# Kernel tuning notes

Hardware: AMD Instinct MI355X
Metric: run time of the kernel (lower is better)

Reference implementation:

```python
import jax, jax.numpy as jnp
import numpy as np

GRID_ROWS, GRID_COLS = 7, 10
GRID_SIZE = GRID_ROWS * GRID_COLS  # 70
CONTEXT_SIZE = 24
STATE_SIZE = GRID_SIZE + CONTEXT_SIZE  # 94
H = 128  # LSTM_HIDDEN


def setup_inputs() -> dict:
    key = jax.random.key(0)
    ks = jax.random.split(key, 16)
    B, T = 1024, 128
    inp = {
        'states_seq': jax.random.normal(ks[0], (B, T, STATE_SIZE), jnp.float32),
        'actions_seq': jax.random.randint(ks[1], (B, T), 0, 4).astype(jnp.int32),
        # conv params (OIHW)
        'conv1_w': jax.random.normal(ks[2], (16, 1, 3, 3), jnp.float32) * 0.3,
        'conv1_b': jnp.zeros((16,), jnp.float32),
        'conv2_w': jax.random.normal(ks[3], (32, 16, 3, 3), jnp.float32) * 0.08,
        'conv2_b': jnp.zeros((32,), jnp.float32),
        # dense params (out, in) like torch Linear
        'grid_fc_w': jax.random.normal(ks[4], (128, 32 * GRID_SIZE), jnp.float32) * 0.02,
        'grid_fc_b': jnp.zeros((128,), jnp.float32),
        'ctx_fc_w': jax.random.normal(ks[5], (64, CONTEXT_SIZE), jnp.float32) * 0.2,
        'ctx_fc_b': jnp.zeros((64,), jnp.float32),
        'trunk_w': jax.random.normal(ks[6], (128, 192), jnp.float32) * 0.07,
        'trunk_b': jnp.zeros((128,), jnp.float32),
        # LSTM params
        'W_ih': jax.random.normal(ks[7], (4 * H, 128), jnp.float32) * 0.09,
        'b_ih': jnp.zeros((4 * H,), jnp.float32),
        'W_hh': jax.random.normal(ks[8], (4 * H, H), jnp.float32) * 0.09,
        # heads
        'actor_w': jax.random.uniform(ks[9], (4, H), jnp.float32, -0.01, 0.01),
        'actor_b': jnp.zeros((4,), jnp.float32),
        'critic_w': jax.random.uniform(ks[10], (1, H), jnp.float32, -0.01, 0.01),
        'critic_b': jnp.zeros((1,), jnp.float32),
    }
    return inp


def _forward(states_seq, actions_seq, conv1_w, conv1_b, conv2_w, conv2_b,
             grid_fc_w, grid_fc_b, ctx_fc_w, ctx_fc_b, trunk_w, trunk_b,
             W_ih, b_ih, W_hh, actor_w, actor_b, critic_w, critic_b):
    B, T, _ = states_seq.shape
    x = states_seq.reshape(-1, STATE_SIZE)                  # (N, 94)
    grid = x[:, :GRID_SIZE].reshape(-1, 1, GRID_ROWS, GRID_COLS)
    ctx = x[:, GRID_SIZE:]
    g = jax.lax.conv_general_dilated(grid, conv1_w, (1, 1), 'SAME',
                                     dimension_numbers=('NCHW', 'OIHW', 'NCHW'))
    g = jax.nn.relu(g + conv1_b[None, :, None, None])
    g = jax.lax.conv_general_dilated(g, conv2_w, (1, 1), 'SAME',
                                     dimension_numbers=('NCHW', 'OIHW', 'NCHW'))
    g = jax.nn.relu(g + conv2_b[None, :, None, None])
    g = g.reshape(g.shape[0], -1)                           # (N, 2240)
    g = jax.nn.relu(g @ grid_fc_w.T + grid_fc_b)            # (N, 128)
    c = jax.nn.relu(ctx @ ctx_fc_w.T + ctx_fc_b)            # (N, 64)
    trunk = jax.nn.relu(jnp.concatenate([g, c], -1) @ trunk_w.T + trunk_b)
    trunk = trunk.reshape(B, T, 128)

    # LSTM: precompute input-to-gate GEMM for all timesteps, scan over time
    gates_x = jnp.einsum('btd,gd->tbg', trunk, W_ih) + b_ih  # (T, B, 4H)

    def step(carry, gx):
        h, cst = carry
        gates = gx + h @ W_hh.T
        i, f, gg, o = jnp.split(gates, 4, axis=-1)
        i, f, o = jax.nn.sigmoid(i), jax.nn.sigmoid(f), jax.nn.sigmoid(o)
        gg = jnp.tanh(gg)
        cst = f * cst + i * gg
        h = o * jnp.tanh(cst)
        return (h, cst), h

    h0 = jnp.zeros((B, H), trunk.dtype)
    _, hs = jax.lax.scan(step, (h0, h0), gates_x)            # hs: (T, B, H)
    h_flat = jnp.transpose(hs, (1, 0, 2)).reshape(B * T, H)

    logits = h_flat @ actor_w.T + actor_b                    # (N, 4)
    values = (h_flat @ critic_w.T + critic_b)[:, 0]          # (N,)
    logp = jax.nn.log_softmax(logits, axis=-1)
    a = actions_seq.reshape(-1)
    log_probs = jnp.take_along_axis(logp, a[:, None].astype(jnp.int32), axis=-1)[:, 0]
    entropy = -jnp.sum(jnp.exp(logp) * logp, axis=-1)
    return log_probs, values, entropy


def reference(states_seq, actions_seq, conv1_w, conv1_b, conv2_w, conv2_b,
              grid_fc_w, grid_fc_b, ctx_fc_w, ctx_fc_b, trunk_w, trunk_b,
              W_ih, b_ih, W_hh, actor_w, actor_b, critic_w, critic_b):
    return _forward(states_seq, actions_seq, conv1_w, conv1_b, conv2_w, conv2_b,
                    grid_fc_w, grid_fc_b, ctx_fc_w, ctx_fc_b, trunk_w, trunk_b,
                    W_ih, b_ih, W_hh, actor_w, actor_b, critic_w, critic_b)
```

## Files before the change

### kernel.cpp

```cpp
#include <hip/hip_runtime.h>
#include <hip/hip_bf16.h>

typedef unsigned int  u32;
typedef unsigned short u16;
typedef unsigned long long u64;
typedef __attribute__((ext_vector_type(8))) short bf16x8;
typedef __attribute__((ext_vector_type(4))) float f32x4;

#define B_   1024
#define T_   128
#define NBT  (B_*T_)
#define CHUNK 32768
#define NCHUNK 4

#define WG_OFF   0
#define WT_OFF   286720
#define WIH_OFF  311296
#define W2_OFF   376832
#define W1C_OFF  381952
#define CVT_TOTAL 382464

#define TRUNK_OFF (1ull<<20)
#define H_OFF     (36ull<<20)
#define CTX_OFF   (72ull<<20)
#define C2_OFF    (92ull<<20)
#define GX_OFF    C2_OFF

__device__ __forceinline__ u16 f2bf(float f){
  __hip_bfloat16 h = __float2bfloat16(f);
  return *reinterpret_cast<u16*>(&h);
}
__device__ __forceinline__ float bf2f(u16 u){ return __uint_as_float((u32)u << 16); }
__device__ __forceinline__ float sigm(float x){ return 1.f / (1.f + __expf(-x)); }
__device__ __forceinline__ float tanh_f(float x){ return 2.f / (1.f + __expf(-2.f*x)) - 1.f; }

__device__ __forceinline__ void bar_lds() {
  __builtin_amdgcn_sched_barrier(0);
  asm volatile("s_waitcnt lgkmcnt(0)" ::: "memory");
  __builtin_amdgcn_s_barrier();
  __builtin_amdgcn_sched_barrier(0);
}

__global__ void k_cvt(const float* __restrict__ gfw, const float* __restrict__ tw,
                      const float* __restrict__ wih, const float* __restrict__ c2w,
                      const float* __restrict__ c1w, u16* __restrict__ wsb) {
  int i = blockIdx.x * 256 + threadIdx.x;
  if (i >= CVT_TOTAL) return;
  float v;
  if (i < WT_OFF) {
    int o = i / 2240; int k = i - o*2240;
    int pos = k >> 5, ch = k & 31;
    v = gfw[o*2240 + ch*70 + pos];
  }
  else if (i < WIH_OFF)  v = tw[i - WT_OFF];
  else if (i < W2_OFF)   v = wih[i - WIH_OFF];
  else if (i < W1C_OFF) {
    int j = i - W2_OFF; int co = j / 160; int k = j - co*160;
    int tap = k >> 4; int ci = k & 15;
    v = (tap < 9) ? c2w[co*144 + ci*9 + tap] : 0.f;
  } else {
    int j = i - W1C_OFF; int ch = j >> 5; int k = j & 31;
    v = (k < 9) ? c1w[ch*9 + k] : 0.f;
  }
  wsb[i] = f2bf(v);
}

__global__ __launch_bounds__(512, 4) void k_conv(
    const float* __restrict__ states,
    const float* __restrict__ c1b, const float* __restrict__ c2b,
    const float* __restrict__ cfw, const float* __restrict__ cfb,
    const u16* __restrict__ wsb,
    u16* __restrict__ c2g,
    u16* __restrict__ ctxg)
{
  __shared__ float s_st[8][96];
  __shared__ __align__(16) u16 act1[8*108*16];

  const int tid  = threadIdx.x;
  const int lane = tid & 63;
  const int w    = tid >> 6;
  const int arow = lane & 15;
  const int grp  = lane >> 4;
  const int g0   = blockIdx.x * 64;

  bf16x8 Bc1 = *(const bf16x8*)(wsb + W1C_OFF + arow*32 + grp*8);
  bf16x8 b2f[5][2];
  #pragma unroll
  for (int p = 0; p < 5; p++)
    #pragma unroll
    for (int nt = 0; nt < 2; nt++)
      b2f[p][nt] = *(const bf16x8*)(wsb + W2_OFF + (nt*16 + arow)*160 + p*32 + grp*8);
  float c1bv[4], c2bv0[4], c2bv1[4];
  #pragma unroll
  for (int r = 0; r < 4; r++) {
    c1bv[r]  = c1b[grp*4 + r];
    c2bv0[r] = c2b[grp*4 + r];
    c2bv1[r] = c2b[16 + grp*4 + r];
  }
  const float cfbr = cfb[lane];
  float cfwr[24];
  #pragma unroll
  for (int k = 0; k < 24; k++) cfwr[k] = cfw[lane*24 + k];

  const int sst_s = (tid*2)/94, sst_c = (tid*2)%94;

  if (tid < 376) {
    float2 v = *(const float2*)(states + (size_t)g0*94 + tid*2);
    *(float2*)&s_st[sst_s][sst_c] = v;
  }
  for (int i = tid; i < 608; i += 512) {
    int s = i / 76; int r = i - s*76; int hi2 = r >> 1; int h = r & 1;
    int hp;
    if (hi2 < 12)      hp = hi2;
    else if (hi2 < 24) hp = 96 + (hi2 - 12);
    else if (hi2 < 31) hp = (hi2 - 23) * 12;
    else               hp = (hi2 - 30) * 12 + 11;
    u32 a = (u32)((s*108 + hp)*32 + h*16) ^ (u32)((hp & 7) << 4);
    *(uint4*)((char*)act1 + a) = (uint4){0,0,0,0};
  }
  bar_lds();

  const bf16x8 zv = {0,0,0,0,0,0,0,0};

  for (int g = 0; g < 8; g++) {
    const int m0 = g0 + g*8;
    float2 npre;
    const bool haspre = (g < 7) && (tid < 376);
    if (haspre)
      npre = *(const float2*)(states + (size_t)(m0 + 8)*94 + tid*2);

    for (int mt = w; mt < 35; mt += 8) {
      int row = mt*16 + arow;
      int s = (int)(((u32)row * 59919u) >> 22); int pos = row - s*70;
      int y = (int)(((u32)pos * 6554u) >> 16);  int x = pos - y*10;
      bf16x8 pf = zv;
      if (grp == 0) {
        const float* gs = &s_st[s][0];
        #pragma unroll
        for (int t = 0; t < 8; t++) {
          int dy = t/3, dx = t - (t/3)*3;
          int yy = y + dy - 1, xx = x + dx - 1;
          bool ok = (yy >= 0) & (yy < 7) & (xx >= 0) & (xx < 10);
          float v = gs[ok ? yy*10 + xx : 0];
          pf[t] = (short)f2bf(ok ? v : 0.f);
        }
      } else if (grp == 1) {
        int yy = y + 1, xx = x + 1;
        bool ok = (yy < 7) & (xx < 10);
        float v = s_st[s][ok ? yy*10 + xx : 0];
        pf[0] = (short)f2bf(ok ? v : 0.f);
      }
      f32x4 acc = __builtin_amdgcn_mfma_f32_16x16x32_bf16(Bc1, pf, (f32x4){0.f,0.f,0.f,0.f}, 0, 0, 0);
      int hp = (y+1)*12 + (x+1);
      u16 q0 = f2bf(fmaxf(acc[0] + c1bv[0], 0.f));
      u16 q1 = f2bf(fmaxf(acc[1] + c1bv[1], 0.f));
      u16 q2 = f2bf(fmaxf(acc[2] + c1bv[2], 0.f));
      u16 q3 = f2bf(fmaxf(acc[3] + c1bv[3], 0.f));
      u64 pk = (u64)q0 | ((u64)q1 << 16) | ((u64)q2 << 32) | ((u64)q3 << 48);
      u32 wa = (u32)(((s*108 + hp)*16 + grp*4)*2) ^ (u32)((hp & 7) << 4);
      *(u64*)((char*)act1 + wa) = pk;
    }
    bar_lds();

    for (int mt = w; mt < 35; mt += 8) {
      int row = mt*16 + arow;
      int s = (int)(((u32)row * 59919u) >> 22); int pos = row - s*70;
      int y = (int)(((u32)pos * 6554u) >> 16);  int x = pos - y*10;
      f32x4 acc0 = {0.f,0.f,0.f,0.f}, acc1 = {0.f,0.f,0.f,0.f};
      #pragma unroll
      for (int p = 0; p < 5; p++) {
        int tap = p*2 + (grp >> 1); if (tap > 8) tap = 8;
        int dy = (tap * 11) >> 5; int dx = tap - dy*3;
        int hp = (y + dy)*12 + (x + dx);
        u32 ra = (u32)(((s*108 + hp)*16 + (grp & 1)*8)*2) ^ (u32)((hp & 7) << 4);
        bf16x8 bv = *(const bf16x8*)((const char*)act1 + ra);
        acc0 = __builtin_amdgcn_mfma_f32_16x16x32_bf16(b2f[p][0], bv, acc0, 0, 0, 0);
        acc1 = __builtin_amdgcn_mfma_f32_16x16x32_bf16(b2f[p][1], bv, acc1, 0, 0, 0);
      }
      {
        u16 q0 = f2bf(fmaxf(acc0[0] + c2bv0[0], 0.f));
        u16 q1 = f2bf(fmaxf(acc0[1] + c2bv0[1], 0.f));
        u16 q2 = f2bf(fmaxf(acc0[2] + c2bv0[2], 0.f));
        u16 q3 = f2bf(fmaxf(acc0[3] + c2bv0[3], 0.f));
        u64 pk = (u64)q0 | ((u64)q1 << 16) | ((u64)q2 << 32) | ((u64)q3 << 48);
        *(u64*)(c2g + (size_t)(m0 + s)*2240 + pos*32 + grp*4) = pk;
      }
      {
        u16 q0 = f2bf(fmaxf(acc1[0] + c2bv1[0], 0.f));
        u16 q1 = f2bf(fmaxf(acc1[1] + c2bv1[1], 0.f));
        u16 q2 = f2bf(fmaxf(acc1[2] + c2bv1[2], 0.f));
        u16 q3 = f2bf(fmaxf(acc1[3] + c2bv1[3], 0.f));
        u64 pk = (u64)q0 | ((u64)q1 << 16) | ((u64)q2 << 32) | ((u64)q3 << 48);
        *(u64*)(c2g + (size_t)(m0 + s)*2240 + pos*32 + 16 + grp*4) = pk;
      }
    }
    {
      float a = cfbr;
      #pragma unroll
      for (int k = 0; k < 24; k++) a = fmaf(cfwr[k], s_st[w][70 + k], a);
      ctxg[(size_t)(m0 + w)*64 + lane] = f2bf(fmaxf(a, 0.f));
    }

    if (g < 7) {
      bar_lds();
      if (haspre) *(float2*)&s_st[sst_s][sst_c] = npre;
      bar_lds();
    }
  }
}

__global__ __launch_bounds__(512, 2) void k_gemm(
    const u16* __restrict__ c2g, const u16* __restrict__ ctxg,
    const float* __restrict__ gfb, const float* __restrict__ tbv,
    const u16* __restrict__ wsb, u16* __restrict__ trunk_ws, int nbase)
{
  __shared__ __align__(16) u16 s_b[2][128*72];
  __shared__ __align__(16) u16 s_g[64*204];

  const int tid  = threadIdx.x;
  const int lane = tid & 63;
  const int w    = tid >> 6;
  const int arow = lane & 15;
  const int grp  = lane >> 4;
  const int wm   = w & 3;
  const int wn   = w >> 2;
  const int m0   = blockIdx.x * 64;

  float gfbv[4], tbvv[4];
  #pragma unroll
  for (int q = 0; q < 4; q++) {
    gfbv[q] = gfb[(wn*4 + q)*16 + arow];
    tbvv[q] = tbv[(wn*4 + q)*16 + arow];
  }

  const int srow = tid >> 2, sseg = (tid & 3) * 16;
  const u16* wg = wsb + WG_OFF;
  const u16* ap = c2g + (size_t)(m0 + wm*16 + arow) * 2240 + grp*8;

  {
    const u16* src = wg + (size_t)srow*2240 + sseg;
    *(uint4*)&s_b[0][srow*72 + sseg]     = *(const uint4*)src;
    *(uint4*)&s_b[0][srow*72 + sseg + 8] = *(const uint4*)(src + 8);
  }
  bf16x8 aC0 = *(const bf16x8*)(ap);
  bf16x8 aC1 = *(const bf16x8*)(ap + 32);
  bf16x8 aN0 = *(const bf16x8*)(ap + 64);
  bf16x8 aN1 = *(const bf16x8*)(ap + 96);
  f32x4 acc[4];
  #pragma unroll
  for (int q = 0; q < 4; q++) acc[q] = (f32x4){0.f,0.f,0.f,0.f};
  __syncthreads();

  for (int kp = 0; kp < 35; kp++) {
    uint4 b0v, b1v;
    if (kp < 34) {
      const u16* src = wg + (size_t)srow*2240 + (kp+1)*64 + sseg;
      b0v = *(const uint4*)src;
      b1v = *(const uint4*)(src + 8);
    }
    bf16x8 aF0 = aN0, aF1 = aN1;
    if (kp < 33) {
      aF0 = *(const bf16x8*)(ap + (size_t)(kp+2)*64);
      aF1 = *(const bf16x8*)(ap + (size_t)(kp+2)*64 + 32);
    }
    const u16* sb = &s_b[kp & 1][0];
    #pragma unroll
    for (int q = 0; q < 4; q++) {
      bf16x8 bv0 = *(const bf16x8*)&sb[((wn*4 + q)*16 + arow)*72 + grp*8];
      acc[q] = __builtin_amdgcn_mfma_f32_16x16x32_bf16(aC0, bv0, acc[q], 0, 0, 0);
    }
    #pragma unroll
    for (int q = 0; q < 4; q++) {
      bf16x8 bv1 = *(const bf16x8*)&sb[((wn*4 + q)*16 + arow)*72 + 32 + grp*8];
      acc[q] = __builtin_amdgcn_mfma_f32_16x16x32_bf16(aC1, bv1, acc[q], 0, 0, 0);
    }
    if (kp < 34) {
      *(uint4*)&s_b[(kp+1) & 1][srow*72 + sseg]     = b0v;
      *(uint4*)&s_b[(kp+1) & 1][srow*72 + sseg + 8] = b1v;
    }
    aC0 = aN0; aC1 = aN1; aN0 = aF0; aN1 = aF1;
    bar_lds();
  }

  #pragma unroll
  for (int q = 0; q < 4; q++)
    #pragma unroll
    for (int r = 0; r < 4; r++)
      s_g[(wm*16 + grp*4 + r)*204 + (wn*4 + q)*16 + arow] = f2bf(fmaxf(acc[q][r] + gfbv[q], 0.f));
  {
    int row = tid >> 3, seg = (tid & 7) * 8;
    uint4 c0 = *(const uint4*)(ctxg + (size_t)(m0 + row)*64 + seg);
    *(uint4*)&s_g[row*204 + 128 + seg] = c0;
  }
  bar_lds();

  f32x4 tacc[4];
  #pragma unroll
  for (int q = 0; q < 4; q++) tacc[q] = (f32x4){0.f,0.f,0.f,0.f};
  #pragma unroll
  for (int ks = 0; ks < 6; ks++) {
    bf16x8 av = *(const bf16x8*)&s_g[(wm*16 + arow)*204 + ks*32 + grp*8];
    #pragma unroll
    for (int q = 0; q < 4; q++) {
      bf16x8 bv = *(const bf16x8*)(wsb + WT_OFF + (size_t)((wn*4 + q)*16 + arow)*192 + ks*32 + grp*8);
      tacc[q] = __builtin_amdgcn_mfma_f32_16x16x32_bf16(av, bv, tacc[q], 0, 0, 0);
    }
  }
  bar_lds();
  #pragma unroll
  for (int q = 0; q < 4; q++)
    #pragma unroll
    for (int r = 0; r < 4; r++)
      s_g[(wm*16 + grp*4 + r)*204 + (wn*4 + q)*16 + arow] = f2bf(fmaxf(tacc[q][r] + tbvv[q], 0.f));
  bar_lds();

  {
    const int t0 = (nbase + m0) & 127;
    const int bb = (nbase + m0) >> 7;
    int row = tid >> 3, seg = (tid & 7) * 16;
    #pragma unroll
    for (int j = 0; j < 2; j++) {
      uint4 v = *(const uint4*)&s_g[row*204 + seg + j*8];
      *(uint4*)(trunk_ws + ((size_t)(t0 + row)*B_ + bb)*128 + seg + j*8) = v;
    }
  }
}

__global__ __launch_bounds__(512, 2) void k_xg(
    const u16* __restrict__ trunk_ws, const u16* __restrict__ wsb,
    u16* __restrict__ gxg)
{
  const int tid  = threadIdx.x;
  const int lane = tid & 63;
  const int w    = tid >> 6;
  const int arow = lane & 15;
  const int grp  = lane >> 4;
  const int t    = blockIdx.x >> 3;
  const int bch  = (blockIdx.x & 7) * 128;
  const int samp = bch + w*16 + arow;

  bf16x8 bv[4];
  #pragma unroll
  for (int ks = 0; ks < 4; ks++)
    bv[ks] = *(const bf16x8*)(trunk_ws + ((size_t)t*B_ + samp)*128 + ks*32 + grp*8);

  const u16* wip = wsb + WIH_OFF;
  u16* gout = gxg + ((size_t)t*B_ + samp)*512;

  #pragma unroll 1
  for (int ntb = 0; ntb < 32; ntb += 4) {
    f32x4 acc[4];
    #pragma unroll
    for (int q = 0; q < 4; q++) acc[q] = (f32x4){0.f,0.f,0.f,0.f};
    #pragma unroll
    for (int ks = 0; ks < 4; ks++) {
      #pragma unroll
      for (int q = 0; q < 4; q++) {
        bf16x8 aw = *(const bf16x8*)(wip + (size_t)((ntb+q)*16 + arow)*128 + ks*32 + grp*8);
        acc[q] = __builtin_amdgcn_mfma_f32_16x16x32_bf16(aw, bv[ks], acc[q], 0, 0, 0);
      }
    }
    #pragma unroll
    for (int q = 0; q < 4; q++) {
      u16 q0 = f2bf(acc[q][0]);
      u16 q1 = f2bf(acc[q][1]);
      u16 q2 = f2bf(acc[q][2]);
      u16 q3 = f2bf(acc[q][3]);
      u64 pk = (u64)q0 | ((u64)q1 << 16) | ((u64)q2 << 32) | ((u64)q3 << 48);
      *(u64*)(gout + (ntb+q)*16 + grp*4) = pk;
    }
  }
}

__global__ __launch_bounds__(512, 1) void k_lstm(
    const u16* __restrict__ gxg, const float* __restrict__ whh,
    const float* __restrict__ bih, u16* __restrict__ h_ws)
{
  __shared__ __align__(16) u16 s_h[2][16*136];

  const int tid  = threadIdx.x;
  const int lane = tid & 63;
  const int w    = tid >> 6;
  const int arow = lane & 15;
  const int grp  = lane >> 4;
  const int b0   = blockIdx.x * 4;

  bf16x8 Bv[4][4];
  float bihv[4];
  #pragma unroll
  for (int j = 0; j < 4; j++) {
    const int row = j*128 + w*16 + arow;
    bihv[j] = bih[row];
    #pragma unroll
    for (int ks = 0; ks < 4; ks++) {
      const float* s1 = whh + (size_t)row*128 + ks*32 + grp*8;
      float4 a0 = *(const float4*)s1, a1 = *(const float4*)(s1 + 4);
      bf16x8 t1;
      t1[0]=(short)f2bf(a0.x); t1[1]=(short)f2bf(a0.y); t1[2]=(short)f2bf(a0.z); t1[3]=(short)f2bf(a0.w);
      t1[4]=(short)f2bf(a1.x); t1[5]=(short)f2bf(a1.y); t1[6]=(short)f2bf(a1.z); t1[7]=(short)f2bf(a1.w);
      Bv[j][ks] = t1;
    }
  }

  for (int i = tid; i < 2*16*136; i += 512) ((u16*)s_h)[i] = 0;

  const u16* gxb = gxg + ((size_t)(b0 + grp))*512 + w*16 + arow;
  u16 Gc[4], Gn[4];
  #pragma unroll
  for (int j = 0; j < 4; j++) {
    Gc[j] = gxb[(size_t)0*B_*512 + j*128];
    Gn[j] = gxb[(size_t)1*B_*512 + j*128];
  }

  const int prow = tid >> 4, pseg = (tid & 15) * 8;
  float cst = 0.f;
  __syncthreads();

  for (int t = 0; t < T_; t++) {
    const int p = t & 1;

    u16 Gf[4] = {0,0,0,0};
    if (t + 2 < T_) {
      #pragma unroll
      for (int j = 0; j < 4; j++)
        Gf[j] = gxb[(size_t)(t+2)*B_*512 + j*128];
    }
    if (t > 0 && tid < 64) {
      uint4 hv = *(const uint4*)&s_h[p][prow*136 + pseg];
      *(uint4*)(h_ws + ((size_t)(t-1)*B_ + b0 + prow)*128 + pseg) = hv;
    }

    f32x4 racc[4];
    #pragma unroll
    for (int j = 0; j < 4; j++) racc[j] = (f32x4){0.f,0.f,0.f,0.f};
    #pragma unroll
    for (int ks = 0; ks < 4; ks++) {
      bf16x8 av = *(const bf16x8*)&s_h[p][arow*136 + ks*32 + grp*8];
      #pragma unroll
      for (int j = 0; j < 4; j++)
        racc[j] = __builtin_amdgcn_mfma_f32_16x16x32_bf16(av, Bv[j][ks], racc[j], 0, 0, 0);
    }

    float g4[4];
    #pragma unroll
    for (int j = 0; j < 4; j++) {
      float t0v = __shfl(racc[j][0], arow);
      float t1v = __shfl(racc[j][1], arow);
      float t2v = __shfl(racc[j][2], arow);
      float t3v = __shfl(racc[j][3], arow);
      g4[j] = (grp == 0) ? t0v : (grp == 1) ? t1v : (grp == 2) ? t2v : t3v;
    }

    {
      float xi = g4[0] + bf2f(Gc[0]) + bihv[0];
      float xf = g4[1] + bf2f(Gc[1]) + bihv[1];
      float xg = g4[2] + bf2f(Gc[2]) + bihv[2];
      float xo = g4[3] + bf2f(Gc[3]) + bihv[3];
      float I = sigm(xi), F = sigm(xf), O = sigm(xo), G = tanh_f(xg);
      cst = F*cst + I*G;
      float hvv = O * tanh_f(cst);
      s_h[1-p][grp*136 + w*16 + arow] = f2bf(hvv);
    }

    #pragma unroll
    for (int j = 0; j < 4; j++) { Gc[j] = Gn[j]; Gn[j] = Gf[j]; }
    bar_lds();
  }

  if (tid < 64) {
    uint4 hv = *(const uint4*)&s_h[T_ & 1][prow*136 + pseg];
    *(uint4*)(h_ws + ((size_t)(T_-1)*B_ + b0 + prow)*128 + pseg) = hv;
  }
}

__global__ __launch_bounds__(256, 1) void k_heads(
    const u16* __restrict__ h_ws, const int* __restrict__ actions,
    const float* __restrict__ aw, const float* __restrict__ ab,
    const float* __restrict__ cw, const float* __restrict__ cb,
    float* __restrict__ out)
{
  const int tid  = threadIdx.x;
  const int lane = tid & 63;
  const int w    = tid >> 6;
  const int arow = lane & 15;
  const int grp  = lane >> 4;

  bf16x8 Ah[4];
  #pragma unroll
  for (int ks = 0; ks < 4; ks++) {
    bf16x8 v = {0,0,0,0,0,0,0,0};
    if (arow < 4) {
      const float* src = aw + arow*128 + ks*32 + grp*8;
      #pragma unroll
      for (int j = 0; j < 8; j++) v[j] = (short)f2bf(src[j]);
    } else if (arow == 4) {
      const float* src = cw + ks*32 + grp*8;
      #pragma unroll
      for (int j = 0; j < 8; j++) v[j] = (short)f2bf(src[j]);
    }
    Ah[ks] = v;
  }
  const float ab0=ab[0], ab1=ab[1], ab2=ab[2], ab3=ab[3], cb0=cb[0];

  #pragma unroll
  for (int g = 0; g < 4; g++) {
    int m0 = (blockIdx.x*4 + w)*64 + g*16;
    int t  = m0 >> 10; int bb = m0 & 1023;
    f32x4 acc = {0.f,0.f,0.f,0.f};
    #pragma unroll
    for (int ks = 0; ks < 4; ks++) {
      bf16x8 bv = *(const bf16x8*)(h_ws + ((size_t)t*B_ + bb + arow)*128 + ks*32 + grp*8);
      acc = __builtin_amdgcn_mfma_f32_16x16x32_bf16(Ah[ks], bv, acc, 0, 0, 0);
    }
    float cr = __shfl_xor(acc[0], 16);
    if (grp == 0) {
      float L0 = acc[0] + ab0, L1 = acc[1] + ab1, L2 = acc[2] + ab2, L3 = acc[3] + ab3;
      float Lv = cr + cb0;
      float mm = fmaxf(fmaxf(L0, L1), fmaxf(L2, L3));
      float e0 = __expf(L0-mm), e1 = __expf(L1-mm), e2 = __expf(L2-mm), e3 = __expf(L3-mm);
      float S = e0+e1+e2+e3; float lse = __logf(S);
      float p0=L0-mm-lse, p1=L1-mm-lse, p2=L2-mm-lse, p3=L3-mm-lse;
      int n = (bb + arow)*T_ + t;
      int a = actions[n];
      float lpa = (a==0)?p0:(a==1)?p1:(a==2)?p2:p3;
      float ent = -(e0*p0 + e1*p1 + e2*p2 + e3*p3) / S;
      out[n] = lpa; out[NBT + n] = Lv; out[2*NBT + n] = ent;
    }
  }
}

extern "C" void kernel_launch(void* const* d_in, const int* in_sizes, int n_in,
                              void* d_out, int out_size, void* d_ws, size_t ws_size,
                              hipStream_t stream) {
  const float* states = (const float*)d_in[0];
  const int*   actions= (const int*)  d_in[1];
  const float* c1w = (const float*)d_in[2];
  const float* c1b = (const float*)d_in[3];
  const float* c2w = (const float*)d_in[4];
  const float* c2b = (const float*)d_in[5];
  const float* gfw = (const float*)d_in[6];
  const float* gfb = (const float*)d_in[7];
  const float* cfw = (const float*)d_in[8];
  const float* cfb = (const float*)d_in[9];
  const float* tw  = (const float*)d_in[10];
  const float* tbv = (const float*)d_in[11];
  const float* wih = (const float*)d_in[12];
  const float* bih = (const float*)d_in[13];
  const float* whh = (const float*)d_in[14];
  const float* aw  = (const float*)d_in[15];
  const float* ab  = (const float*)d_in[16];
  const float* cw  = (const float*)d_in[17];
  const float* cb  = (const float*)d_in[18];
  float* out = (float*)d_out;

  u16* wsb   = (u16*)d_ws;
  u16* trunk = (u16*)((char*)d_ws + TRUNK_OFF);
  u16* h_ws  = (u16*)((char*)d_ws + H_OFF);
  u16* ctxg  = (u16*)((char*)d_ws + CTX_OFF);
  u16* c2g   = (u16*)((char*)d_ws + C2_OFF);
  u16* gxg   = (u16*)((char*)d_ws + GX_OFF);

  k_cvt<<<(CVT_TOTAL + 255)/256, 256, 0, stream>>>(gfw, tw, wih, c2w, c1w, wsb);

  for (int c = 0; c < NCHUNK; c++) {
    const float* st_c = states + (size_t)c * CHUNK * 94;
    u16* ctx_c = ctxg + (size_t)c * CHUNK * 64;
    k_conv<<<CHUNK/64, 512, 0, stream>>>(st_c, c1b, c2b, cfw, cfb, wsb, c2g, ctx_c);
    k_gemm<<<CHUNK/64, 512, 0, stream>>>(c2g, ctx_c, gfb, tbv, wsb, trunk, c*CHUNK);
  }
  k_xg<<<T_*8, 512, 0, stream>>>(trunk, wsb, gxg);
  k_lstm<<<B_/4, 512, 0, stream>>>(gxg, whh, bih, h_ws);
  k_heads<<<512, 256, 0, stream>>>(h_ws, actions, aw, ab, cw, cb, out);
}
```

Before: 791.4 us.

## Fuse input-gate projection into LSTM recurrence, drop separate xg kernel

Removes the k_xg kernel that precomputed W_ih·x for every timestep into a bf16 buffer of about 128 MB. The LSTM kernel now holds W_ih in registers and computes next-step input gates with extra MFMAs inside the recurrence loop. A 3-slot LDS ring is fed by register prefetch of trunk rows several steps ahead. This removes the large global write and readback, but adds MFMA work and register pressure to the serial recurrent loop, and it pads each 16-row MFMA with 4 repeated batch rows.

```diff
diff --git a/kernel.cpp b/kernel.cpp
--- a/kernel.cpp
+++ b/kernel.cpp
@@ -24,7 +24,6 @@
 #define H_OFF     (36ull<<20)
 #define CTX_OFF   (72ull<<20)
 #define C2_OFF    (92ull<<20)
-#define GX_OFF    C2_OFF
 
 __device__ __forceinline__ u16 f2bf(float f){
   __hip_bfloat16 h = __float2bfloat16(f);
@@ -326,57 +325,13 @@
   }
 }
 
-__global__ __launch_bounds__(512, 2) void k_xg(
-    const u16* __restrict__ trunk_ws, const u16* __restrict__ wsb,
-    u16* __restrict__ gxg)
-{
-  const int tid  = threadIdx.x;
-  const int lane = tid & 63;
-  const int w    = tid >> 6;
-  const int arow = lane & 15;
-  const int grp  = lane >> 4;
-  const int t    = blockIdx.x >> 3;
-  const int bch  = (blockIdx.x & 7) * 128;
-  const int samp = bch + w*16 + arow;
-
-  bf16x8 bv[4];
-  #pragma unroll
-  for (int ks = 0; ks < 4; ks++)
-    bv[ks] = *(const bf16x8*)(trunk_ws + ((size_t)t*B_ + samp)*128 + ks*32 + grp*8);
-
-  const u16* wip = wsb + WIH_OFF;
-  u16* gout = gxg + ((size_t)t*B_ + samp)*512;
-
-  #pragma unroll 1
-  for (int ntb = 0; ntb < 32; ntb += 4) {
-    f32x4 acc[4];
-    #pragma unroll
-    for (int q = 0; q < 4; q++) acc[q] = (f32x4){0.f,0.f,0.f,0.f};
-    #pragma unroll
-    for (int ks = 0; ks < 4; ks++) {
-      #pragma unroll
-      for (int q = 0; q < 4; q++) {
-        bf16x8 aw = *(const bf16x8*)(wip + (size_t)((ntb+q)*16 + arow)*128 + ks*32 + grp*8);
-        acc[q] = __builtin_amdgcn_mfma_f32_16x16x32_bf16(aw, bv[ks], acc[q], 0, 0, 0);
-      }
-    }
-    #pragma unroll
-    for (int q = 0; q < 4; q++) {
-      u16 q0 = f2bf(acc[q][0]);
-      u16 q1 = f2bf(acc[q][1]);
-      u16 q2 = f2bf(acc[q][2]);
-      u16 q3 = f2bf(acc[q][3]);
-      u64 pk = (u64)q0 | ((u64)q1 << 16) | ((u64)q2 << 32) | ((u64)q3 << 48);
-      *(u64*)(gout + (ntb+q)*16 + grp*4) = pk;
-    }
-  }
-}
-
 __global__ __launch_bounds__(512, 1) void k_lstm(
-    const u16* __restrict__ gxg, const float* __restrict__ whh,
-    const float* __restrict__ bih, u16* __restrict__ h_ws)
+    const u16* __restrict__ trunk_ws, const float* __restrict__ whh,
+    const float* __restrict__ wih, const float* __restrict__ bih,
+    u16* __restrict__ h_ws)
 {
   __shared__ __align__(16) u16 s_h[2][16*136];
+  __shared__ __align__(16) u16 s_tk[3][4*136];
 
   const int tid  = threadIdx.x;
   const int lane = tid & 63;
@@ -385,7 +340,7 @@
   const int grp  = lane >> 4;
   const int b0   = blockIdx.x * 4;
 
-  bf16x8 Bv[4][4];
+  bf16x8 Bv[4][4], Bw[4][4];
   float bihv[4];
   #pragma unroll
   for (int j = 0; j < 4; j++) {
@@ -394,45 +349,60 @@
     #pragma unroll
     for (int ks = 0; ks < 4; ks++) {
       const float* s1 = whh + (size_t)row*128 + ks*32 + grp*8;
+      const float* s2 = wih + (size_t)row*128 + ks*32 + grp*8;
       float4 a0 = *(const float4*)s1, a1 = *(const float4*)(s1 + 4);
-      bf16x8 t1;
+      float4 b0v = *(const float4*)s2, b1v = *(const float4*)(s2 + 4);
+      bf16x8 t1, t2;
       t1[0]=(short)f2bf(a0.x); t1[1]=(short)f2bf(a0.y); t1[2]=(short)f2bf(a0.z); t1[3]=(short)f2bf(a0.w);
       t1[4]=(short)f2bf(a1.x); t1[5]=(short)f2bf(a1.y); t1[6]=(short)f2bf(a1.z); t1[7]=(short)f2bf(a1.w);
-      Bv[j][ks] = t1;
+      t2[0]=(short)f2bf(b0v.x); t2[1]=(short)f2bf(b0v.y); t2[2]=(short)f2bf(b0v.z); t2[3]=(short)f2bf(b0v.w);
+      t2[4]=(short)f2bf(b1v.x); t2[5]=(short)f2bf(b1v.y); t2[6]=(short)f2bf(b1v.z); t2[7]=(short)f2bf(b1v.w);
+      Bv[j][ks] = t1; Bw[j][ks] = t2;
     }
   }
 
   for (int i = tid; i < 2*16*136; i += 512) ((u16*)s_h)[i] = 0;
 
-  const u16* gxb = gxg + ((size_t)(b0 + grp))*512 + w*16 + arow;
-  u16 Gc[4], Gn[4];
-  #pragma unroll
-  for (int j = 0; j < 4; j++) {
-    Gc[j] = gxb[(size_t)0*B_*512 + j*128];
-    Gn[j] = gxb[(size_t)1*B_*512 + j*128];
-  }
-
   const int prow = tid >> 4, pseg = (tid & 15) * 8;
+  if (tid < 64) {
+    #pragma unroll
+    for (int s = 0; s < 3; s++)
+      *(uint4*)&s_tk[s][prow*136 + pseg] =
+          *(const uint4*)(trunk_ws + ((size_t)s*B_ + b0 + prow)*128 + pseg);
+  }
+  uint4 P0 = {0,0,0,0};
+  if (tid < 64)
+    P0 = *(const uint4*)(trunk_ws + ((size_t)3*B_ + b0 + prow)*128 + pseg);
+
   float cst = 0.f;
   __syncthreads();
 
+  f32x4 xA[4];
+  #pragma unroll
+  for (int j = 0; j < 4; j++) xA[j] = (f32x4){0.f,0.f,0.f,0.f};
+  #pragma unroll
+  for (int ks = 0; ks < 4; ks++) {
+    bf16x8 av = *(const bf16x8*)&s_tk[0][(arow & 3)*136 + ks*32 + grp*8];
+    #pragma unroll
+    for (int j = 0; j < 4; j++)
+      xA[j] = __builtin_amdgcn_mfma_f32_16x16x32_bf16(av, Bw[j][ks], xA[j], 0, 0, 0);
+  }
+
   for (int t = 0; t < T_; t++) {
     const int p = t & 1;
 
-    u16 Gf[4] = {0,0,0,0};
-    if (t + 2 < T_) {
-      #pragma unroll
-      for (int j = 0; j < 4; j++)
-        Gf[j] = gxb[(size_t)(t+2)*B_*512 + j*128];
-    }
+    uint4 P1 = {0,0,0,0};
+    if ((t + 4 < T_) && tid < 64)
+      P1 = *(const uint4*)(trunk_ws + ((size_t)(t+4)*B_ + b0 + prow)*128 + pseg);
+
     if (t > 0 && tid < 64) {
       uint4 hv = *(const uint4*)&s_h[p][prow*136 + pseg];
       *(uint4*)(h_ws + ((size_t)(t-1)*B_ + b0 + prow)*128 + pseg) = hv;
     }
 
-    f32x4 racc[4];
-    #pragma unroll
-    for (int j = 0; j < 4; j++) racc[j] = (f32x4){0.f,0.f,0.f,0.f};
+    f32x4 racc[4], xB[4];
+    #pragma unroll
+    for (int j = 0; j < 4; j++) { racc[j] = (f32x4){0.f,0.f,0.f,0.f}; xB[j] = (f32x4){0.f,0.f,0.f,0.f}; }
     #pragma unroll
     for (int ks = 0; ks < 4; ks++) {
       bf16x8 av = *(const bf16x8*)&s_h[p][arow*136 + ks*32 + grp*8];
@@ -440,30 +410,47 @@
       for (int j = 0; j < 4; j++)
         racc[j] = __builtin_amdgcn_mfma_f32_16x16x32_bf16(av, Bv[j][ks], racc[j], 0, 0, 0);
     }
+    {
+      const u16* tk = &s_tk[(t+1) % 3][0];
+      #pragma unroll
+      for (int ks = 0; ks < 4; ks++) {
+        bf16x8 av = *(const bf16x8*)&tk[(arow & 3)*136 + ks*32 + grp*8];
+        #pragma unroll
+        for (int j = 0; j < 4; j++)
+          xB[j] = __builtin_amdgcn_mfma_f32_16x16x32_bf16(av, Bw[j][ks], xB[j], 0, 0, 0);
+      }
+    }
 
     float g4[4];
     #pragma unroll
     for (int j = 0; j < 4; j++) {
-      float t0v = __shfl(racc[j][0], arow);
-      float t1v = __shfl(racc[j][1], arow);
-      float t2v = __shfl(racc[j][2], arow);
-      float t3v = __shfl(racc[j][3], arow);
+      float s0 = racc[j][0] + xA[j][0];
+      float s1 = racc[j][1] + xA[j][1];
+      float s2 = racc[j][2] + xA[j][2];
+      float s3 = racc[j][3] + xA[j][3];
+      float t0v = __shfl(s0, arow);
+      float t1v = __shfl(s1, arow);
+      float t2v = __shfl(s2, arow);
+      float t3v = __shfl(s3, arow);
       g4[j] = (grp == 0) ? t0v : (grp == 1) ? t1v : (grp == 2) ? t2v : t3v;
     }
 
     {
-      float xi = g4[0] + bf2f(Gc[0]) + bihv[0];
-      float xf = g4[1] + bf2f(Gc[1]) + bihv[1];
-      float xg = g4[2] + bf2f(Gc[2]) + bihv[2];
-      float xo = g4[3] + bf2f(Gc[3]) + bihv[3];
+      float xi = g4[0] + bihv[0];
+      float xf = g4[1] + bihv[1];
+      float xg = g4[2] + bihv[2];
+      float xo = g4[3] + bihv[3];
       float I = sigm(xi), F = sigm(xf), O = sigm(xo), G = tanh_f(xg);
       cst = F*cst + I*G;
       float hvv = O * tanh_f(cst);
       s_h[1-p][grp*136 + w*16 + arow] = f2bf(hvv);
     }
 
-    #pragma unroll
-    for (int j = 0; j < 4; j++) { Gc[j] = Gn[j]; Gn[j] = Gf[j]; }
+    if ((t + 3 < T_) && tid < 64)
+      *(uint4*)&s_tk[t % 3][prow*136 + pseg] = P0;
+    P0 = P1;
+    #pragma unroll
+    for (int j = 0; j < 4; j++) xA[j] = xB[j];
     bar_lds();
   }
 
@@ -558,7 +545,6 @@
   u16* h_ws  = (u16*)((char*)d_ws + H_OFF);
   u16* ctxg  = (u16*)((char*)d_ws + CTX_OFF);
   u16* c2g   = (u16*)((char*)d_ws + C2_OFF);
-  u16* gxg   = (u16*)((char*)d_ws + GX_OFF);
 
   k_cvt<<<(CVT_TOTAL + 255)/256, 256, 0, stream>>>(gfw, tw, wih, c2w, c1w, wsb);
 
@@ -568,7 +554,6 @@
     k_conv<<<CHUNK/64, 512, 0, stream>>>(st_c, c1b, c2b, cfw, cfb, wsb, c2g, ctx_c);
     k_gemm<<<CHUNK/64, 512, 0, stream>>>(c2g, ctx_c, gfb, tbv, wsb, trunk, c*CHUNK);
   }
-  k_xg<<<T_*8, 512, 0, stream>>>(trunk, wsb, gxg);
-  k_lstm<<<B_/4, 512, 0, stream>>>(gxg, whh, bih, h_ws);
+  k_lstm<<<B_/4, 512, 0, stream>>>(trunk, whh, wih, bih, h_ws);
   k_heads<<<512, 256, 0, stream>>>(h_ws, actions, aw, ab, cw, cb, out);
 }
```

After: 690.3 us (median of 2 runs). -12.8%, faster.
